# Kernel tuning notes

Hardware: AMD Instinct MI355X
Metric: run time of the kernel (lower is better)

The kernel has to match this reference:

```python
import jax, jax.numpy as jnp
import numpy as np

N_HEAD = 16


def _rope(x, cos, sin):
    # x: [B, T, H, hd]; cos/sin: [1, T, 1, hd//2] (interleaved-pair rotation)
    x1, x2 = x[..., ::2], x[..., 1::2]
    r1 = x1 * cos - x2 * sin
    r2 = x1 * sin + x2 * cos
    return jnp.stack([r1, r2], axis=-1).reshape(x.shape)


def setup_inputs() -> dict:
    key = jax.random.key(0)
    k1, k2, k3 = jax.random.split(key, 3)
    B, T, D = 2, 2048, 2048
    x = jax.random.normal(k1, (B, T, D), dtype=jnp.float32)
    w_attn = jax.random.normal(k2, (3 * D, D), dtype=jnp.float32) * 0.02
    w_proj = jax.random.normal(k3, (D, D), dtype=jnp.float32) * 0.02
    return {"x": x, "w_attn": w_attn, "w_proj": w_proj}


def reference(x, w_attn, w_proj):
    B, T, D = x.shape
    H = N_HEAD
    hd = D // H
    # fused QKV projection (bias=False)
    qkv = x @ w_attn.T                      # [B, T, 3D]
    q, k, v = jnp.split(qkv, 3, axis=-1)
    q = q.reshape(B, T, H, hd)
    k = k.reshape(B, T, H, hd)
    v = v.reshape(B, T, H, hd)
    # RoPE tables: inv_freq = 1/10000^(2i/hd), angles m*theta_i
    inv_freq = 1.0 / (10000.0 ** (jnp.arange(0, hd, 2, dtype=jnp.float32) / hd))
    t = jnp.arange(T, dtype=jnp.float32)
    freqs = t[:, None] * inv_freq[None, :]  # [T, hd//2]
    cos = jnp.cos(freqs)[None, :, None, :]
    sin = jnp.sin(freqs)[None, :, None, :]
    q = _rope(q, cos, sin)
    k = _rope(k, cos, sin)
    # causal attention with materialized [B,H,T,T] scores (as in source)
    scale = 1.0 / np.sqrt(hd).astype(np.float32)
    att = jnp.einsum('bthd,bshd->bhts', q, k) * scale
    causal = jnp.tril(jnp.ones((T, T), dtype=bool))
    att = jnp.where(causal, att, -jnp.inf)
    att = jax.nn.softmax(att, axis=-1)
    y = jnp.einsum('bhts,bshd->bthd', att, v).reshape(B, T, D)
    return y @ w_proj.T
```

## Files before the change

### kernel.cpp

```cpp
#include <hip/hip_runtime.h>
#include <hip/hip_bf16.h>

#define T_SEQ 2048
#define DMODEL 2048
#define NB 2
#define NH 16
#define HD 128

typedef __attribute__((ext_vector_type(8))) short short8;
typedef __attribute__((ext_vector_type(4))) float f32x4;
typedef __attribute__((ext_vector_type(16))) float f32x16;
typedef unsigned short ushort_t;

__device__ inline ushort_t f2bf(float f) {
  union { float f; unsigned u; } v; v.f = f;
  unsigned r = v.u + 0x7fffu + ((v.u >> 16) & 1u);
  return (ushort_t)(r >> 16);
}
__device__ inline float bf2f(ushort_t u) {
  union { unsigned u; float f; } v; v.u = ((unsigned)u) << 16;
  return v.f;
}
__device__ inline unsigned pk2(float x, float y) {
  union { __hip_bfloat162 h; unsigned u; } c;
  c.h = __float22bfloat162_rn(float2{x, y});
  return c.u;
}
__device__ inline float fexp2(float x) {
  float r;
  asm("v_exp_f32 %0, %1" : "=v"(r) : "v"(x));
  return r;
}

__device__ inline void gload16(const void* g, void* l) {
  __builtin_amdgcn_global_load_lds(
      (const __attribute__((address_space(1))) unsigned*)g,
      (__attribute__((address_space(3))) unsigned*)l, 16, 0, 0);
}

__global__ void cvt_f32_bf16(const float* __restrict__ src, ushort_t* __restrict__ dst, int n8) {
  int i = blockIdx.x * blockDim.x + threadIdx.x;
  if (i >= n8) return;
  const float4* s = (const float4*)src + (size_t)i * 2;
  float4 a = s[0], b = s[1];
  short8 o;
  o[0] = (short)f2bf(a.x); o[1] = (short)f2bf(a.y);
  o[2] = (short)f2bf(a.z); o[3] = (short)f2bf(a.w);
  o[4] = (short)f2bf(b.x); o[5] = (short)f2bf(b.y);
  o[6] = (short)f2bf(b.z); o[7] = (short)f2bf(b.w);
  *((short8*)dst + i) = o;
}

__global__ void trig_init(float* __restrict__ trig) {
  int idx = blockIdx.x * blockDim.x + threadIdx.x;
  if (idx >= T_SEQ * 64) return;
  int i = idx & 63, t = idx >> 6;
  float inv = __expf(-(float)i * (9.210340371976184f / 64.0f));
  float f = (float)t * inv;
  trig[idx * 2]     = cosf(f);
  trig[idx * 2 + 1] = sinf(f);
}

template <int EPI>
__global__ __launch_bounds__(256)
void gemm_bt(const ushort_t* __restrict__ A, const ushort_t* __restrict__ Bt,
             float* __restrict__ C, ushort_t* __restrict__ q_t,
             ushort_t* __restrict__ k_t, ushort_t* __restrict__ vt,
             const float* __restrict__ trig, int M, int N, int K) {
  __shared__ __align__(16) ushort_t smem[8192];
  ushort_t* As = smem;
  ushort_t* Bs = smem + 4096;
  int tid = threadIdx.x, lane = tid & 63, w = tid >> 6;
  int wm = w >> 1, wn = w & 1;
  int li = lane & 15, lg = lane >> 4;
  int tile_n = blockIdx.x * 128, tile_m = blockIdx.y * 128;
  f32x4 acc[4][4] = {};
  int arow = lane >> 2, acol = (lane & 3) * 8;
  const ushort_t* Ag = A + (size_t)tile_m * K;
  const ushort_t* Bg = Bt + (size_t)tile_n * K;
  for (int k0 = 0; k0 < K; k0 += 32) {
#pragma unroll
    for (int i = 0; i < 2; ++i) {
      int blk = w * 2 + i;
      gload16(Ag + (size_t)(blk * 16 + arow) * K + k0 + acol, &As[blk * 512]);
      gload16(Bg + (size_t)(blk * 16 + arow) * K + k0 + acol, &Bs[blk * 512]);
    }
    __syncthreads();
    short8 af[4], bfr[4];
#pragma unroll
    for (int mi = 0; mi < 4; ++mi)
      af[mi] = *(const short8*)&As[(wm * 64 + mi * 16 + li) * 32 + lg * 8];
#pragma unroll
    for (int ni = 0; ni < 4; ++ni)
      bfr[ni] = *(const short8*)&Bs[(wn * 64 + ni * 16 + li) * 32 + lg * 8];
#pragma unroll
    for (int mi = 0; mi < 4; ++mi)
#pragma unroll
      for (int ni = 0; ni < 4; ++ni)
        acc[mi][ni] = __builtin_amdgcn_mfma_f32_16x16x32_bf16(af[mi], bfr[ni], acc[mi][ni], 0, 0, 0);
    __syncthreads();
  }

  if (EPI == 0) {
#pragma unroll
    for (int mi = 0; mi < 4; ++mi) {
      int row = tile_m + wm * 64 + mi * 16 + lg * 4;
#pragma unroll
      for (int ni = 0; ni < 4; ++ni) {
        int col = tile_n + wn * 64 + ni * 16 + li;
#pragma unroll
        for (int r = 0; r < 4; ++r)
          C[(size_t)(row + r) * N + col] = acc[mi][ni][r];
      }
    }
  } else {
    int sec = tile_n >> 11;
    int nn  = tile_n & 2047;
    int h   = nn >> 7;
    int bq  = tile_m >> 11;
    int t0  = tile_m & 2047;
    if (sec < 2) {
      ushort_t* dst = (sec == 0) ? q_t : k_t;
      ushort_t* base = dst + ((size_t)(bq * NH + h)) * T_SEQ * HD;
#pragma unroll
      for (int mi = 0; mi < 4; ++mi) {
        int tl = wm * 64 + mi * 16 + lg * 4;
#pragma unroll
        for (int ni = 0; ni < 4; ++ni) {
          int d = wn * 64 + ni * 16 + li;
          int fi = d >> 1;
#pragma unroll
          for (int r = 0; r < 4; ++r) {
            int t = t0 + tl + r;
            float val = acc[mi][ni][r];
            float par = __shfl_xor(val, 1);
            const float* tp = trig + t * 128 + fi * 2;
            float c = tp[0], s = tp[1];
            float out = (li & 1) ? (par * s + val * c) : (val * c - par * s);
            base[(size_t)t * HD + d] = f2bf(out);
          }
        }
      }
    } else {
      ushort_t* vbase = vt + ((size_t)(bq * NH + h)) * HD * T_SEQ;
#pragma unroll
      for (int c = 0; c < 2; ++c) {
        __syncthreads();
        if (wm == c) {
#pragma unroll
          for (int mi = 0; mi < 4; ++mi)
#pragma unroll
            for (int ni = 0; ni < 4; ++ni) {
              int d = wn * 64 + ni * 16 + li;
#pragma unroll
              for (int r = 0; r < 4; ++r) {
                int tl = mi * 16 + lg * 4 + r;
                smem[d * 64 + (tl ^ ((d & 7) << 3))] = f2bf(acc[mi][ni][r]);
              }
            }
        }
        __syncthreads();
#pragma unroll
        for (int j = 0; j < 4; ++j) {
          int idx = j * 256 + tid;
          int d = idx >> 3, tg = idx & 7;
          short8 val = *(const short8*)&smem[d * 64 + ((tg * 8) ^ ((d & 7) << 3))];
          *(short8*)(vbase + (size_t)d * T_SEQ + t0 + c * 64 + tg * 8) = val;
        }
      }
    }
  }
}

__global__ __launch_bounds__(256, 2)
void flash_attn(const ushort_t* __restrict__ Q, const ushort_t* __restrict__ Kg,
                const ushort_t* __restrict__ Vt, ushort_t* __restrict__ Y) {
  __shared__ __align__(16) ushort_t ldsK[2 * 64 * 128];
  __shared__ __align__(16) ushort_t ldsV[2 * 128 * 64];
  int tid = threadIdx.x, lane = tid & 63, w = tid >> 6;
  int hi = lane >> 5, l31 = lane & 31;
  int qi = (blockIdx.y & 16) ? (15 - (int)blockIdx.x) : (int)blockIdx.x;
  int bh = blockIdx.y;
  int b = bh >> 4, h = bh & 15;
  int q0 = qi * 128;
  const ushort_t* Qp = Q + (size_t)bh * T_SEQ * HD;
  const ushort_t* Kp = Kg + (size_t)bh * T_SEQ * HD;
  const ushort_t* Vp = Vt + (size_t)bh * HD * T_SEQ;

  int qg = q0 + w * 32 + l31;
  int qmaxw = q0 + w * 32 + 31;

  auto stage = [&](int kv0, int bsel) {
    ushort_t* Kb = ldsK + bsel * 8192;
    ushort_t* Vb = ldsV + bsel * 8192;
#pragma unroll
    for (int p = 0; p < 4; ++p) {
      int c = p * 256 + w * 64 + lane;
      {
        int row = c >> 4, cc = c & 15;
        int sc = cc ^ (row & 15);
        gload16(Kp + (size_t)(kv0 + row) * HD + sc * 8, Kb + (p * 256 + w * 64) * 8);
      }
      {
        int d = c >> 3, cc = c & 7;
        int sc = cc ^ (d & 7);
        gload16(Vp + (size_t)d * T_SEQ + kv0 + sc * 8, Vb + (p * 256 + w * 64) * 8);
      }
    }
  };

  short8 qf[8];
#pragma unroll
  for (int ds = 0; ds < 8; ++ds)
    qf[ds] = *(const short8*)(Qp + (size_t)qg * HD + ds * 16 + hi * 8);

  f32x16 o[4] = {};
  float mu = -1e30f, l = 0.f;
  const float SIG = 0.12751879523209784f;

  int nkt = 2 * qi + 2;
  stage(0, 0);
  __syncthreads();
  int cur = 0;
  for (int kt = 0; kt < nkt; ++kt) {
    int kv0 = kt * 64;
    if (kt + 1 < nkt) stage((kt + 1) * 64, cur ^ 1);
    if (kv0 <= qmaxw) {
      const ushort_t* Kb = ldsK + cur * 8192;
      const ushort_t* Vb = ldsV + cur * 8192;
      f32x16 sa = {}, sb = {};
      __builtin_amdgcn_s_setprio(1);
#pragma unroll
      for (int ds = 0; ds < 8; ++ds) {
        int cc = ds * 2 + hi;
        short8 k0 = *(const short8*)&Kb[l31 * 128 + ((cc ^ (l31 & 15)) * 8)];
        short8 k1 = *(const short8*)&Kb[(32 + l31) * 128 + ((cc ^ (l31 & 15)) * 8)];
        sa = __builtin_amdgcn_mfma_f32_32x32x16_bf16(k0, qf[ds], sa, 0, 0, 0);
        sb = __builtin_amdgcn_mfma_f32_32x32x16_bf16(k1, qf[ds], sb, 0, 0, 0);
      }
      __builtin_amdgcn_s_setprio(0);
      float p[32];
#pragma unroll
      for (int r = 0; r < 16; ++r) { p[r] = sa[r] * SIG; p[16 + r] = sb[r] * SIG; }
      if (kv0 + 63 > q0 + w * 32) {
#pragma unroll
        for (int r = 0; r < 16; ++r) {
          int loc = (r & 3) + 8 * (r >> 2) + 4 * hi;
          if (kv0 + loc > qg)      p[r]      = -3e38f;
          if (kv0 + 32 + loc > qg) p[16 + r] = -3e38f;
        }
      }
      float tm[16];
#pragma unroll
      for (int i = 0; i < 16; ++i) tm[i] = fmaxf(p[i], p[i + 16]);
#pragma unroll
      for (int st = 8; st >= 1; st >>= 1)
#pragma unroll
        for (int i = 0; i < 8; ++i)
          if (i < st) tm[i] = fmaxf(tm[i], tm[i + st]);
      float pmax = fmaxf(tm[0], __shfl_xor(tm[0], 32));
      bool resc = !__all(pmax <= mu + 11.0f);
      if (resc) {
        float munew = fmaxf(mu, pmax);
        float alpha = fexp2(mu - munew);
        mu = munew;
        l *= alpha;
#pragma unroll
        for (int dsub = 0; dsub < 4; ++dsub)
#pragma unroll
          for (int r = 0; r < 16; ++r) o[dsub][r] *= alpha;
      }
#pragma unroll
      for (int i = 0; i < 32; ++i) p[i] = fexp2(p[i] - mu);
      float ts[16];
#pragma unroll
      for (int i = 0; i < 16; ++i) ts[i] = p[i] + p[i + 16];
#pragma unroll
      for (int st = 8; st >= 1; st >>= 1)
#pragma unroll
        for (int i = 0; i < 8; ++i)
          if (i < st) ts[i] += ts[i + st];
      l += ts[0] + __shfl_xor(ts[0], 32);
      __builtin_amdgcn_s_setprio(1);
#pragma unroll
      for (int s = 0; s < 4; ++s) {
        int rb = (s >> 1) * 16 + (s & 1) * 8;
        unsigned a0 = pk2(p[rb + 0], p[rb + 1]);
        unsigned a1 = pk2(p[rb + 2], p[rb + 3]);
        unsigned a2 = pk2(p[rb + 4], p[rb + 5]);
        unsigned a3 = pk2(p[rb + 6], p[rb + 7]);
        unsigned sa0 = (unsigned)__shfl_xor((int)a0, 32);
        unsigned sa1 = (unsigned)__shfl_xor((int)a1, 32);
        unsigned sa2 = (unsigned)__shfl_xor((int)a2, 32);
        unsigned sa3 = (unsigned)__shfl_xor((int)a3, 32);
        union { unsigned u[4]; short8 s8; } pf;
        pf.u[0] = hi ? sa2 : a0;
        pf.u[1] = hi ? sa3 : a1;
        pf.u[2] = hi ? a2 : sa0;
        pf.u[3] = hi ? a3 : sa1;
#pragma unroll
        for (int dsub = 0; dsub < 4; ++dsub) {
          int row = dsub * 32 + l31;
          short8 vf = *(const short8*)&Vb[row * 64 + (((2 * s + hi) ^ (row & 7)) * 8)];
          o[dsub] = __builtin_amdgcn_mfma_f32_32x32x16_bf16(vf, pf.s8, o[dsub], 0, 0, 0);
        }
      }
      __builtin_amdgcn_s_setprio(0);
    }
    __syncthreads();
    cur ^= 1;
  }
  float invl = 1.f / l;
#pragma unroll
  for (int dsub = 0; dsub < 4; ++dsub)
#pragma unroll
    for (int r = 0; r < 16; ++r) o[dsub][r] *= invl;
#pragma unroll
  for (int dsub = 0; dsub < 4; ++dsub)
#pragma unroll
    for (int r = 0; r < 16; r += 2) {
      int d0 = dsub * 32 + (r & 3) + 8 * (r >> 2) + 4 * hi;
      unsigned u = pk2(o[dsub][r], o[dsub][r + 1]);
      *(unsigned*)&ldsK[w * 4096 + l31 * 128 + (((d0 >> 3) ^ (l31 & 15)) * 8) + (d0 & 7)] = u;
    }
  __syncthreads();
#pragma unroll
  for (int rep = 0; rep < 8; ++rep) {
    int idx = rep * 256 + tid;
    int qg2 = idx >> 4, c = idx & 15;
    int wv2 = qg2 >> 5, ql = qg2 & 31;
    short8 val = *(const short8*)&ldsK[wv2 * 4096 + ql * 128 + ((c ^ (ql & 15)) * 8)];
    *(short8*)(Y + ((size_t)(b * T_SEQ + q0 + qg2)) * DMODEL + h * HD + c * 8) = val;
  }
}

extern "C" void kernel_launch(void* const* d_in, const int* in_sizes, int n_in,
                              void* d_out, int out_size, void* d_ws, size_t ws_size,
                              hipStream_t stream) {
  const float* x      = (const float*)d_in[0];
  const float* w_attn = (const float*)d_in[1];
  const float* w_proj = (const float*)d_in[2];
  float* out = (float*)d_out;

  char* ws = (char*)d_ws;
  size_t off = 0;
  auto alloc = [&](size_t bytes) -> void* {
    void* p = ws + off;
    off = (off + bytes + 255) & ~(size_t)255;
    return p;
  };
  const size_t MT = (size_t)NB * T_SEQ;
  ushort_t* xb   = (ushort_t*)alloc(MT * DMODEL * 2);
  ushort_t* wab  = (ushort_t*)alloc((size_t)3 * DMODEL * DMODEL * 2);
  ushort_t* wpb  = (ushort_t*)alloc((size_t)DMODEL * DMODEL * 2);
  ushort_t* q_t  = (ushort_t*)alloc(MT * DMODEL * 2);
  ushort_t* k_t  = (ushort_t*)alloc(MT * DMODEL * 2);
  ushort_t* vtb  = (ushort_t*)alloc(MT * DMODEL * 2);
  ushort_t* yb   = (ushort_t*)alloc(MT * DMODEL * 2);
  float*    trig = (float*)alloc((size_t)T_SEQ * 64 * 2 * 4);
  (void)ws_size; (void)n_in; (void)in_sizes; (void)out_size;

  {
    int n8x = (int)(MT * DMODEL / 8);
    hipLaunchKernelGGL(cvt_f32_bf16, dim3((n8x + 255) / 256), dim3(256), 0, stream, x, xb, n8x);
    int n8a = (int)((size_t)3 * DMODEL * DMODEL / 8);
    hipLaunchKernelGGL(cvt_f32_bf16, dim3((n8a + 255) / 256), dim3(256), 0, stream, w_attn, wab, n8a);
    int n8p = (int)((size_t)DMODEL * DMODEL / 8);
    hipLaunchKernelGGL(cvt_f32_bf16, dim3((n8p + 255) / 256), dim3(256), 0, stream, w_proj, wpb, n8p);
  }
  hipLaunchKernelGGL(trig_init, dim3(T_SEQ * 64 / 256), dim3(256), 0, stream, trig);

  hipLaunchKernelGGL((gemm_bt<1>), dim3(3 * DMODEL / 128, MT / 128), dim3(256), 0, stream,
                     xb, wab, (float*)nullptr, q_t, k_t, vtb, trig,
                     (int)MT, 3 * DMODEL, DMODEL);

  hipLaunchKernelGGL(flash_attn, dim3(T_SEQ / 128, NB * NH), dim3(256), 0, stream,
                     q_t, k_t, vtb, yb);

  hipLaunchKernelGGL((gemm_bt<0>), dim3(DMODEL / 128, MT / 128), dim3(256), 0, stream,
                     yb, wpb, out, (ushort_t*)nullptr, (ushort_t*)nullptr, (ushort_t*)nullptr,
                     (const float*)nullptr, (int)MT, DMODEL, DMODEL);
}
```

Measured before the change: 317.8 us.

## Replace GEMMs with 256x256 double-buffered swizzled LDS kernel and separate V transpose

Replaces the 128x128, BK=32 single-buffered GEMM with a 512-thread 256x256 tile kernel using BK=64, XOR-swizzled LDS, double buffering with prefetch of the next K tile interleaved into the MFMA phases, and s_setprio around MFMA bursts. The V section of the QKV epilogue now writes row-major V, and a new transpose kernel produces the transposed V layout flash attention expects. The aim is more reuse per global load, fewer bank conflicts, and loads overlapped with compute. The cost is an extra kernel launch, an extra round trip of V through memory, and a much larger LDS footprint per block. The output GEMM has only 64 blocks, which may underfill the GPU.

```diff
diff --git a/kernel.cpp b/kernel.cpp
--- a/kernel.cpp
+++ b/kernel.cpp
@@ -6,6 +6,7 @@
 #define NB 2
 #define NH 16
 #define HD 128
+#define BK 64
 
 typedef __attribute__((ext_vector_type(8))) short short8;
 typedef __attribute__((ext_vector_type(4))) float f32x4;
@@ -61,111 +62,155 @@
   trig[idx * 2 + 1] = sinf(f);
 }
 
+__global__ __launch_bounds__(256)
+void v_transpose(const ushort_t* __restrict__ v, ushort_t* __restrict__ vt) {
+  __shared__ __align__(16) ushort_t L[64][136];
+  int bh = blockIdx.y;
+  int t0 = blockIdx.x * 64;
+  int tid = threadIdx.x;
+  int row = tid >> 2, c0 = (tid & 3) * 32;
+  const ushort_t* src = v + ((size_t)bh * T_SEQ + t0 + row) * HD + c0;
+#pragma unroll
+  for (int j = 0; j < 4; ++j)
+    *(short8*)&L[row][c0 + j * 8] = *(const short8*)(src + j * 8);
+  __syncthreads();
+  int d = tid >> 1, tc = (tid & 1) * 32;
+  union { ushort_t u[32]; short8 v8[4]; } buf;
+#pragma unroll
+  for (int j = 0; j < 32; ++j) buf.u[j] = L[tc + j][d];
+  ushort_t* dst = vt + ((size_t)bh * HD + d) * T_SEQ + t0 + tc;
+#pragma unroll
+  for (int j = 0; j < 4; ++j) *(short8*)(dst + j * 8) = buf.v8[j];
+}
+
 template <int EPI>
-__global__ __launch_bounds__(256)
-void gemm_bt(const ushort_t* __restrict__ A, const ushort_t* __restrict__ Bt,
+__global__ __launch_bounds__(512, 2)
+void gemm256(const ushort_t* __restrict__ A, const ushort_t* __restrict__ Bt,
              float* __restrict__ C, ushort_t* __restrict__ q_t,
-             ushort_t* __restrict__ k_t, ushort_t* __restrict__ vt,
+             ushort_t* __restrict__ k_t, ushort_t* __restrict__ v_t,
              const float* __restrict__ trig, int M, int N, int K) {
-  __shared__ __align__(16) ushort_t smem[8192];
-  ushort_t* As = smem;
-  ushort_t* Bs = smem + 4096;
+  __shared__ __align__(16) ushort_t sA[2][256 * 64];
+  __shared__ __align__(16) ushort_t sB[2][256 * 64];
   int tid = threadIdx.x, lane = tid & 63, w = tid >> 6;
-  int wm = w >> 1, wn = w & 1;
+  int wm = w >> 2, wn = w & 3;
   int li = lane & 15, lg = lane >> 4;
-  int tile_n = blockIdx.x * 128, tile_m = blockIdx.y * 128;
-  f32x4 acc[4][4] = {};
-  int arow = lane >> 2, acol = (lane & 3) * 8;
+  int tile_m = blockIdx.y * 256, tile_n = blockIdx.x * 256;
   const ushort_t* Ag = A + (size_t)tile_m * K;
   const ushort_t* Bg = Bt + (size_t)tile_n * K;
-  for (int k0 = 0; k0 < K; k0 += 32) {
+
+  int srow = w * 16 + (lane >> 3);
+  int schunk = ((lane & 7) ^ (lane >> 3)) * 8;
+
+  auto stageA = [&](int half, int kt, int buf) {
 #pragma unroll
     for (int i = 0; i < 2; ++i) {
-      int blk = w * 2 + i;
-      gload16(Ag + (size_t)(blk * 16 + arow) * K + k0 + acol, &As[blk * 512]);
-      gload16(Bg + (size_t)(blk * 16 + arow) * K + k0 + acol, &Bs[blk * 512]);
-    }
-    __syncthreads();
-    short8 af[4], bfr[4];
-#pragma unroll
-    for (int mi = 0; mi < 4; ++mi)
-      af[mi] = *(const short8*)&As[(wm * 64 + mi * 16 + li) * 32 + lg * 8];
-#pragma unroll
-    for (int ni = 0; ni < 4; ++ni)
-      bfr[ni] = *(const short8*)&Bs[(wn * 64 + ni * 16 + li) * 32 + lg * 8];
-#pragma unroll
-    for (int mi = 0; mi < 4; ++mi)
-#pragma unroll
-      for (int ni = 0; ni < 4; ++ni)
-        acc[mi][ni] = __builtin_amdgcn_mfma_f32_16x16x32_bf16(af[mi], bfr[ni], acc[mi][ni], 0, 0, 0);
-    __syncthreads();
+      int row = half * 128 + srow + i * 8;
+      gload16(Ag + (size_t)row * K + kt * BK + schunk,
+              &sA[buf][half * 8192 + w * 1024 + i * 512]);
+    }
+  };
+  auto stageB = [&](int half, int kt, int buf) {
+#pragma unroll
+    for (int i = 0; i < 2; ++i) {
+      int row = half * 128 + srow + i * 8;
+      gload16(Bg + (size_t)row * K + kt * BK + schunk,
+              &sB[buf][half * 8192 + w * 1024 + i * 512]);
+    }
+  };
+
+  f32x4 acc[8][4] = {};
+  short8 bfr[4][2];
+  const int NT = K / BK;
+
+  stageA(0, 0, 0); stageA(1, 0, 0); stageB(0, 0, 0); stageB(1, 0, 0);
+  asm volatile("s_waitcnt vmcnt(0)" ::: "memory");
+  __syncthreads();
+
+  for (int kt = 0; kt < NT; ++kt) {
+    int cur = kt & 1;
+    bool pref = (kt + 1 < NT);
+#pragma unroll
+    for (int p = 0; p < 4; ++p) {
+      short8 af[2][2];
+#pragma unroll
+      for (int mm = 0; mm < 2; ++mm) {
+        int row = wm * 128 + (p * 2 + mm) * 16 + li;
+#pragma unroll
+        for (int kh = 0; kh < 2; ++kh)
+          af[mm][kh] = *(const short8*)&sA[cur][row * 64 + (((kh * 4 + lg) ^ (row & 7)) * 8)];
+      }
+      if (p == 0) {
+#pragma unroll
+        for (int n = 0; n < 4; ++n) {
+          int row = wn * 64 + n * 16 + li;
+#pragma unroll
+          for (int kh = 0; kh < 2; ++kh)
+            bfr[n][kh] = *(const short8*)&sB[cur][row * 64 + (((kh * 4 + lg) ^ (row & 7)) * 8)];
+        }
+      }
+      if (pref) {
+        if (p == 0) { stageA(0, kt + 1, cur ^ 1); stageB(0, kt + 1, cur ^ 1); }
+        else if (p == 1) { stageA(1, kt + 1, cur ^ 1); stageB(1, kt + 1, cur ^ 1); }
+      }
+      __builtin_amdgcn_s_barrier();
+      asm volatile("s_waitcnt lgkmcnt(0)" ::: "memory");
+      __builtin_amdgcn_sched_barrier(0);
+      __builtin_amdgcn_s_setprio(1);
+#pragma unroll
+      for (int mm = 0; mm < 2; ++mm)
+#pragma unroll
+        for (int n = 0; n < 4; ++n)
+#pragma unroll
+          for (int kh = 0; kh < 2; ++kh)
+            acc[p * 2 + mm][n] = __builtin_amdgcn_mfma_f32_16x16x32_bf16(
+                af[mm][kh], bfr[n][kh], acc[p * 2 + mm][n], 0, 0, 0);
+      __builtin_amdgcn_s_setprio(0);
+      if (p == 3) asm volatile("s_waitcnt vmcnt(0)" ::: "memory");
+      __builtin_amdgcn_s_barrier();
+    }
   }
 
   if (EPI == 0) {
 #pragma unroll
-    for (int mi = 0; mi < 4; ++mi) {
-      int row = tile_m + wm * 64 + mi * 16 + lg * 4;
-#pragma unroll
-      for (int ni = 0; ni < 4; ++ni) {
-        int col = tile_n + wn * 64 + ni * 16 + li;
+    for (int m = 0; m < 8; ++m) {
+      int trow = tile_m + wm * 128 + m * 16 + lg * 4;
+#pragma unroll
+      for (int n = 0; n < 4; ++n) {
+        int col = tile_n + wn * 64 + n * 16 + li;
 #pragma unroll
         for (int r = 0; r < 4; ++r)
-          C[(size_t)(row + r) * N + col] = acc[mi][ni][r];
+          C[(size_t)(trow + r) * N + col] = acc[m][n][r];
       }
     }
   } else {
     int sec = tile_n >> 11;
-    int nn  = tile_n & 2047;
-    int h   = nn >> 7;
     int bq  = tile_m >> 11;
     int t0  = tile_m & 2047;
-    if (sec < 2) {
-      ushort_t* dst = (sec == 0) ? q_t : k_t;
-      ushort_t* base = dst + ((size_t)(bq * NH + h)) * T_SEQ * HD;
-#pragma unroll
-      for (int mi = 0; mi < 4; ++mi) {
-        int tl = wm * 64 + mi * 16 + lg * 4;
-#pragma unroll
-        for (int ni = 0; ni < 4; ++ni) {
-          int d = wn * 64 + ni * 16 + li;
-          int fi = d >> 1;
+#pragma unroll
+    for (int m = 0; m < 8; ++m) {
+      int tl = wm * 128 + m * 16 + lg * 4;
+#pragma unroll
+      for (int n = 0; n < 4; ++n) {
+        int nn = (tile_n & 2047) + wn * 64 + n * 16 + li;
+        int h = nn >> 7, d = nn & 127;
+        if (sec < 2) {
+          ushort_t* base = ((sec == 0) ? q_t : k_t) + ((size_t)(bq * NH + h)) * T_SEQ * HD;
+          int fi2 = (d >> 1) * 2;
 #pragma unroll
           for (int r = 0; r < 4; ++r) {
             int t = t0 + tl + r;
-            float val = acc[mi][ni][r];
+            float val = acc[m][n][r];
             float par = __shfl_xor(val, 1);
-            const float* tp = trig + t * 128 + fi * 2;
+            const float* tp = trig + t * 128 + fi2;
             float c = tp[0], s = tp[1];
-            float out = (li & 1) ? (par * s + val * c) : (val * c - par * s);
-            base[(size_t)t * HD + d] = f2bf(out);
+            float outv = (li & 1) ? (par * s + val * c) : (val * c - par * s);
+            base[(size_t)t * HD + d] = f2bf(outv);
           }
-        }
-      }
-    } else {
-      ushort_t* vbase = vt + ((size_t)(bq * NH + h)) * HD * T_SEQ;
-#pragma unroll
-      for (int c = 0; c < 2; ++c) {
-        __syncthreads();
-        if (wm == c) {
-#pragma unroll
-          for (int mi = 0; mi < 4; ++mi)
-#pragma unroll
-            for (int ni = 0; ni < 4; ++ni) {
-              int d = wn * 64 + ni * 16 + li;
-#pragma unroll
-              for (int r = 0; r < 4; ++r) {
-                int tl = mi * 16 + lg * 4 + r;
-                smem[d * 64 + (tl ^ ((d & 7) << 3))] = f2bf(acc[mi][ni][r]);
-              }
-            }
-        }
-        __syncthreads();
-#pragma unroll
-        for (int j = 0; j < 4; ++j) {
-          int idx = j * 256 + tid;
-          int d = idx >> 3, tg = idx & 7;
-          short8 val = *(const short8*)&smem[d * 64 + ((tg * 8) ^ ((d & 7) << 3))];
-          *(short8*)(vbase + (size_t)d * T_SEQ + t0 + c * 64 + tg * 8) = val;
+        } else {
+          ushort_t* base = v_t + ((size_t)(bq * NH + h)) * T_SEQ * HD;
+#pragma unroll
+          for (int r = 0; r < 4; ++r)
+            base[(size_t)(t0 + tl + r) * HD + d] = f2bf(acc[m][n][r]);
         }
       }
     }
@@ -355,6 +400,7 @@
   ushort_t* wpb  = (ushort_t*)alloc((size_t)DMODEL * DMODEL * 2);
   ushort_t* q_t  = (ushort_t*)alloc(MT * DMODEL * 2);
   ushort_t* k_t  = (ushort_t*)alloc(MT * DMODEL * 2);
+  ushort_t* v_t  = (ushort_t*)alloc(MT * DMODEL * 2);
   ushort_t* vtb  = (ushort_t*)alloc(MT * DMODEL * 2);
   ushort_t* yb   = (ushort_t*)alloc(MT * DMODEL * 2);
   float*    trig = (float*)alloc((size_t)T_SEQ * 64 * 2 * 4);
@@ -370,14 +416,16 @@
   }
   hipLaunchKernelGGL(trig_init, dim3(T_SEQ * 64 / 256), dim3(256), 0, stream, trig);
 
-  hipLaunchKernelGGL((gemm_bt<1>), dim3(3 * DMODEL / 128, MT / 128), dim3(256), 0, stream,
-                     xb, wab, (float*)nullptr, q_t, k_t, vtb, trig,
+  hipLaunchKernelGGL((gemm256<1>), dim3(3 * DMODEL / 256, MT / 256), dim3(512), 0, stream,
+                     xb, wab, (float*)nullptr, q_t, k_t, v_t, trig,
                      (int)MT, 3 * DMODEL, DMODEL);
+
+  hipLaunchKernelGGL(v_transpose, dim3(T_SEQ / 64, NB * NH), dim3(256), 0, stream, v_t, vtb);
 
   hipLaunchKernelGGL(flash_attn, dim3(T_SEQ / 128, NB * NH), dim3(256), 0, stream,
                      q_t, k_t, vtb, yb);
 
-  hipLaunchKernelGGL((gemm_bt<0>), dim3(DMODEL / 128, MT / 128), dim3(256), 0, stream,
+  hipLaunchKernelGGL((gemm256<0>), dim3(DMODEL / 256, MT / 256), dim3(512), 0, stream,
                      yb, wpb, out, (ushort_t*)nullptr, (ushort_t*)nullptr, (ushort_t*)nullptr,
                      (const float*)nullptr, (int)MT, DMODEL, DMODEL);
 }
```

New measurement: 300.4 us. 5.5% less time.

## Double-buffer GEMM with 256x128 tiles, swizzled LDS, and separate V transpose kernel

Applied to the files above, without the earlier changes.

Replaces the single-buffered 128x128 GEMM with a 512-thread, 256x128-tile kernel that double-buffers LDS, so the next K-slice loads while the current one computes. It applies an XOR swizzle to cut LDS bank conflicts and raises MFMA priority with s_setprio. The V transpose moves out of the QKV GEMM epilogue into a separate kernel through an extra workspace buffer. This adds a launch and an extra pass over V in exchange for a simpler, more uniform epilogue.

```diff
diff --git a/kernel.cpp b/kernel.cpp
--- a/kernel.cpp
+++ b/kernel.cpp
@@ -61,111 +61,129 @@
   trig[idx * 2 + 1] = sinf(f);
 }
 
+__global__ __launch_bounds__(256)
+void v_transpose(const ushort_t* __restrict__ v, ushort_t* __restrict__ vt) {
+  __shared__ __align__(16) ushort_t L[64][136];
+  int bh = blockIdx.y;
+  int t0 = blockIdx.x * 64;
+  int tid = threadIdx.x;
+  int row = tid >> 2, c0 = (tid & 3) * 32;
+  const ushort_t* src = v + ((size_t)bh * T_SEQ + t0 + row) * HD + c0;
+#pragma unroll
+  for (int j = 0; j < 4; ++j)
+    *(short8*)&L[row][c0 + j * 8] = *(const short8*)(src + j * 8);
+  __syncthreads();
+  int d = tid >> 1, tc = (tid & 1) * 32;
+  union { ushort_t u[32]; short8 v8[4]; } buf;
+#pragma unroll
+  for (int j = 0; j < 32; ++j) buf.u[j] = L[tc + j][d];
+  ushort_t* dst = vt + ((size_t)bh * HD + d) * T_SEQ + t0 + tc;
+#pragma unroll
+  for (int j = 0; j < 4; ++j) *(short8*)(dst + j * 8) = buf.v8[j];
+}
+
 template <int EPI>
-__global__ __launch_bounds__(256)
-void gemm_bt(const ushort_t* __restrict__ A, const ushort_t* __restrict__ Bt,
-             float* __restrict__ C, ushort_t* __restrict__ q_t,
-             ushort_t* __restrict__ k_t, ushort_t* __restrict__ vt,
-             const float* __restrict__ trig, int M, int N, int K) {
-  __shared__ __align__(16) ushort_t smem[8192];
-  ushort_t* As = smem;
-  ushort_t* Bs = smem + 4096;
+__global__ __launch_bounds__(512, 4)
+void gemm_s(const ushort_t* __restrict__ A, const ushort_t* __restrict__ Bt,
+            float* __restrict__ C, ushort_t* __restrict__ q_t,
+            ushort_t* __restrict__ k_t, ushort_t* __restrict__ v_t,
+            const float* __restrict__ trig, int M, int N, int K) {
+  __shared__ __align__(16) ushort_t sA[2][256 * 32];
+  __shared__ __align__(16) ushort_t sB[2][128 * 32];
   int tid = threadIdx.x, lane = tid & 63, w = tid >> 6;
   int wm = w >> 1, wn = w & 1;
   int li = lane & 15, lg = lane >> 4;
-  int tile_n = blockIdx.x * 128, tile_m = blockIdx.y * 128;
-  f32x4 acc[4][4] = {};
-  int arow = lane >> 2, acol = (lane & 3) * 8;
+  int tile_m = blockIdx.y * 256, tile_n = blockIdx.x * 128;
   const ushort_t* Ag = A + (size_t)tile_m * K;
   const ushort_t* Bg = Bt + (size_t)tile_n * K;
-  for (int k0 = 0; k0 < K; k0 += 32) {
+
+  int srow = tid >> 2;
+  int sc0  = tid & 3;
+
+  auto swz = [](int r, int c) { return c ^ (r & 3) ^ ((r >> 2) & 3); };
+
+  auto stage = [&](int kt, int buf) {
 #pragma unroll
     for (int i = 0; i < 2; ++i) {
-      int blk = w * 2 + i;
-      gload16(Ag + (size_t)(blk * 16 + arow) * K + k0 + acol, &As[blk * 512]);
-      gload16(Bg + (size_t)(blk * 16 + arow) * K + k0 + acol, &Bs[blk * 512]);
-    }
-    __syncthreads();
-    short8 af[4], bfr[4];
+      int row = i * 128 + srow;
+      gload16(Ag + (size_t)row * K + kt * 32 + swz(row, sc0) * 8,
+              &sA[buf][i * 4096 + tid * 8]);
+    }
+    gload16(Bg + (size_t)srow * K + kt * 32 + swz(srow, sc0) * 8,
+            &sB[buf][tid * 8]);
+  };
+
+  f32x4 acc[4][4] = {};
+  const int NT = K / 32;
+
+  stage(0, 0);
+  __syncthreads();
+
+  for (int kt = 0; kt < NT; ++kt) {
+    int cur = kt & 1;
+    if (kt + 1 < NT) stage(kt + 1, cur ^ 1);
+    short8 af[4], bf[4];
+#pragma unroll
+    for (int mi = 0; mi < 4; ++mi) {
+      int row = wm * 64 + mi * 16 + li;
+      af[mi] = *(const short8*)&sA[cur][row * 32 + swz(row, lg) * 8];
+    }
+#pragma unroll
+    for (int ni = 0; ni < 4; ++ni) {
+      int row = wn * 64 + ni * 16 + li;
+      bf[ni] = *(const short8*)&sB[cur][row * 32 + swz(row, lg) * 8];
+    }
+    __builtin_amdgcn_s_setprio(1);
 #pragma unroll
     for (int mi = 0; mi < 4; ++mi)
-      af[mi] = *(const short8*)&As[(wm * 64 + mi * 16 + li) * 32 + lg * 8];
-#pragma unroll
-    for (int ni = 0; ni < 4; ++ni)
-      bfr[ni] = *(const short8*)&Bs[(wn * 64 + ni * 16 + li) * 32 + lg * 8];
-#pragma unroll
-    for (int mi = 0; mi < 4; ++mi)
 #pragma unroll
       for (int ni = 0; ni < 4; ++ni)
-        acc[mi][ni] = __builtin_amdgcn_mfma_f32_16x16x32_bf16(af[mi], bfr[ni], acc[mi][ni], 0, 0, 0);
+        acc[mi][ni] = __builtin_amdgcn_mfma_f32_16x16x32_bf16(af[mi], bf[ni], acc[mi][ni], 0, 0, 0);
+    __builtin_amdgcn_s_setprio(0);
     __syncthreads();
   }
 
   if (EPI == 0) {
 #pragma unroll
     for (int mi = 0; mi < 4; ++mi) {
-      int row = tile_m + wm * 64 + mi * 16 + lg * 4;
+      int trow = tile_m + wm * 64 + mi * 16 + lg * 4;
 #pragma unroll
       for (int ni = 0; ni < 4; ++ni) {
         int col = tile_n + wn * 64 + ni * 16 + li;
 #pragma unroll
         for (int r = 0; r < 4; ++r)
-          C[(size_t)(row + r) * N + col] = acc[mi][ni][r];
+          C[(size_t)(trow + r) * N + col] = acc[mi][ni][r];
       }
     }
   } else {
     int sec = tile_n >> 11;
-    int nn  = tile_n & 2047;
-    int h   = nn >> 7;
     int bq  = tile_m >> 11;
     int t0  = tile_m & 2047;
-    if (sec < 2) {
-      ushort_t* dst = (sec == 0) ? q_t : k_t;
-      ushort_t* base = dst + ((size_t)(bq * NH + h)) * T_SEQ * HD;
-#pragma unroll
-      for (int mi = 0; mi < 4; ++mi) {
-        int tl = wm * 64 + mi * 16 + lg * 4;
-#pragma unroll
-        for (int ni = 0; ni < 4; ++ni) {
-          int d = wn * 64 + ni * 16 + li;
-          int fi = d >> 1;
+    int h   = (tile_n & 2047) >> 7;
+#pragma unroll
+    for (int mi = 0; mi < 4; ++mi) {
+      int tl = wm * 64 + mi * 16 + lg * 4;
+#pragma unroll
+      for (int ni = 0; ni < 4; ++ni) {
+        int d = wn * 64 + ni * 16 + li;
+        if (sec < 2) {
+          ushort_t* base = ((sec == 0) ? q_t : k_t) + ((size_t)(bq * NH + h)) * T_SEQ * HD;
+          int fi2 = (d >> 1) * 2;
 #pragma unroll
           for (int r = 0; r < 4; ++r) {
             int t = t0 + tl + r;
             float val = acc[mi][ni][r];
             float par = __shfl_xor(val, 1);
-            const float* tp = trig + t * 128 + fi * 2;
+            const float* tp = trig + t * 128 + fi2;
             float c = tp[0], s = tp[1];
-            float out = (li & 1) ? (par * s + val * c) : (val * c - par * s);
-            base[(size_t)t * HD + d] = f2bf(out);
+            float outv = (li & 1) ? (par * s + val * c) : (val * c - par * s);
+            base[(size_t)t * HD + d] = f2bf(outv);
           }
-        }
-      }
-    } else {
-      ushort_t* vbase = vt + ((size_t)(bq * NH + h)) * HD * T_SEQ;
-#pragma unroll
-      for (int c = 0; c < 2; ++c) {
-        __syncthreads();
-        if (wm == c) {
-#pragma unroll
-          for (int mi = 0; mi < 4; ++mi)
-#pragma unroll
-            for (int ni = 0; ni < 4; ++ni) {
-              int d = wn * 64 + ni * 16 + li;
-#pragma unroll
-              for (int r = 0; r < 4; ++r) {
-                int tl = mi * 16 + lg * 4 + r;
-                smem[d * 64 + (tl ^ ((d & 7) << 3))] = f2bf(acc[mi][ni][r]);
-              }
-            }
-        }
-        __syncthreads();
-#pragma unroll
-        for (int j = 0; j < 4; ++j) {
-          int idx = j * 256 + tid;
-          int d = idx >> 3, tg = idx & 7;
-          short8 val = *(const short8*)&smem[d * 64 + ((tg * 8) ^ ((d & 7) << 3))];
-          *(short8*)(vbase + (size_t)d * T_SEQ + t0 + c * 64 + tg * 8) = val;
+        } else {
+          ushort_t* base = v_t + ((size_t)(bq * NH + h)) * T_SEQ * HD;
+#pragma unroll
+          for (int r = 0; r < 4; ++r)
+            base[(size_t)(t0 + tl + r) * HD + d] = f2bf(acc[mi][ni][r]);
         }
       }
     }
@@ -355,6 +373,7 @@
   ushort_t* wpb  = (ushort_t*)alloc((size_t)DMODEL * DMODEL * 2);
   ushort_t* q_t  = (ushort_t*)alloc(MT * DMODEL * 2);
   ushort_t* k_t  = (ushort_t*)alloc(MT * DMODEL * 2);
+  ushort_t* v_t  = (ushort_t*)alloc(MT * DMODEL * 2);
   ushort_t* vtb  = (ushort_t*)alloc(MT * DMODEL * 2);
   ushort_t* yb   = (ushort_t*)alloc(MT * DMODEL * 2);
   float*    trig = (float*)alloc((size_t)T_SEQ * 64 * 2 * 4);
@@ -370,14 +389,16 @@
   }
   hipLaunchKernelGGL(trig_init, dim3(T_SEQ * 64 / 256), dim3(256), 0, stream, trig);
 
-  hipLaunchKernelGGL((gemm_bt<1>), dim3(3 * DMODEL / 128, MT / 128), dim3(256), 0, stream,
-                     xb, wab, (float*)nullptr, q_t, k_t, vtb, trig,
+  hipLaunchKernelGGL((gemm_s<1>), dim3(3 * DMODEL / 128, MT / 256), dim3(512), 0, stream,
+                     xb, wab, (float*)nullptr, q_t, k_t, v_t, trig,
                      (int)MT, 3 * DMODEL, DMODEL);
+
+  hipLaunchKernelGGL(v_transpose, dim3(T_SEQ / 64, NB * NH), dim3(256), 0, stream, v_t, vtb);
 
   hipLaunchKernelGGL(flash_attn, dim3(T_SEQ / 128, NB * NH), dim3(256), 0, stream,
                      q_t, k_t, vtb, yb);
 
-  hipLaunchKernelGGL((gemm_bt<0>), dim3(DMODEL / 128, MT / 128), dim3(256), 0, stream,
+  hipLaunchKernelGGL((gemm_s<0>), dim3(DMODEL / 128, MT / 256), dim3(512), 0, stream,
                      yb, wpb, out, (ushort_t*)nullptr, (ushort_t*)nullptr, (ushort_t*)nullptr,
                      (const float*)nullptr, (int)MT, DMODEL, DMODEL);
 }
```

Measured after the change: 310.0 us. -2.5%, faster.
